# Kernel optimization log

Measured on AMD Instinct MI355X. Metric: run time of the kernel, lower is better.

## Reference

```python
import jax, jax.numpy as jnp
import numpy as np

V, E, S, B, T = 100000, 64, 4, 2048, 200
D = 2 * E          # memory_vector_dim
C = E              # controller_units
CIN = 2 * E + D    # controller input: x_t (2E) + prev read (D)
P = 2 * (D + 1) + 2 * D  # (key+beta) for read & write heads + erase + add


def setup_inputs() -> dict:
    key = jax.random.key(0)
    ks = jax.random.split(key, 16)
    g = lambda k, sh, sc=0.05: jax.random.normal(k, sh, dtype=jnp.float32) * sc
    return {
        "item": jax.random.randint(ks[0], (B,), 0, V),
        "cate": jax.random.randint(ks[1], (B,), 0, V),
        "hist_item": jax.random.randint(ks[2], (B, T), 0, V),
        "hist_cate": jax.random.randint(ks[3], (B, T), 0, V),
        "mask": jnp.ones((B, T), jnp.float32),
        "embedding": g(ks[4], (V, E)),
        "gru_Wih": g(ks[5], (3 * C, CIN)),
        "gru_Whh": g(ks[6], (3 * C, C)),
        "gru_bih": jnp.zeros((3 * C,), jnp.float32),
        "gru_bhh": jnp.zeros((3 * C,), jnp.float32),
        "Wp": g(ks[7], (P, C)),
        "bp": jnp.zeros((P,), jnp.float32),
        "Wo": g(ks[8], (E, C + D)),
        "bo": jnp.zeros((E,), jnp.float32),
        "M0": g(ks[9], (S, D), 0.1),
        "fc1_w": g(ks[10], (200, 5 * E)),
        "fc1_b": jnp.zeros((200,), jnp.float32),
        "prelu1_a": jnp.full((1,), 0.25, jnp.float32),
        "fc2_w": g(ks[11], (80, 200)),
        "fc2_b": jnp.zeros((80,), jnp.float32),
        "prelu2_a": jnp.full((1,), 0.25, jnp.float32),
        "fc3_w": g(ks[12], (2, 80)),
        "fc3_b": jnp.zeros((2,), jnp.float32),
    }


def _cos_addr(k, beta, M):
    # content addressing: softmax(beta * cosine_sim(k, M))  k:[B,D] M:[B,S,D]
    kn = k / (jnp.linalg.norm(k, axis=-1, keepdims=True) + 1e-8)
    Mn = M / (jnp.linalg.norm(M, axis=-1, keepdims=True) + 1e-8)
    K = jnp.einsum('bd,bsd->bs', kn, Mn)
    return jax.nn.softmax(beta[:, None] * K, axis=-1)


def _prelu(x, a):
    return jnp.where(x > 0, x, a * x)


def _mimn_rnn(hist_emb, mask, gru_Wih, gru_Whh, gru_bih, gru_bhh, Wp, bp, Wo, bo, M0):
    Bn = hist_emb.shape[0]
    h0 = jnp.zeros((Bn, C), hist_emb.dtype)
    r0 = jnp.zeros((Bn, D), hist_emb.dtype)
    Mi = jnp.broadcast_to(M0[None], (Bn, S, D))

    def step(carry, inp):
        h, M, read = carry
        x_t, m_t = inp                      # x_t [B,2E], m_t [B]
        ctrl_in = jnp.concatenate([x_t, read], axis=-1)
        gi = ctrl_in @ gru_Wih.T + gru_bih
        gh = h @ gru_Whh.T + gru_bhh
        i_r, i_z, i_n = jnp.split(gi, 3, axis=-1)
        h_r, h_z, h_n = jnp.split(gh, 3, axis=-1)
        rg = jax.nn.sigmoid(i_r + h_r)
        zg = jax.nn.sigmoid(i_z + h_z)
        ng = jnp.tanh(i_n + rg * h_n)
        h_new = (1.0 - zg) * ng + zg * h
        # head parameters
        p = h_new @ Wp.T + bp               # [B, P]
        hp_r, hp_w = p[:, :D + 1], p[:, D + 1:2 * (D + 1)]
        erase = jax.nn.sigmoid(p[:, 2 * (D + 1):2 * (D + 1) + D])
        add = jnp.tanh(p[:, -D:])
        k_r, beta_r = jnp.tanh(hp_r[:, :D]), jax.nn.softplus(hp_r[:, D])
        k_w, beta_w = jnp.tanh(hp_w[:, :D]), jax.nn.softplus(hp_w[:, D])
        w_r = _cos_addr(k_r, beta_r, M)
        w_w = _cos_addr(k_w, beta_w, M)
        read_new = jnp.einsum('bs,bsd->bd', w_r, M)
        M_new = M * (1.0 - w_w[..., None] * erase[:, None, :]) + w_w[..., None] * add[:, None, :]
        out = jnp.concatenate([h_new, read_new], axis=-1) @ Wo.T + bo  # [B,E]
        # sequence-length masking (dynamic_rnn semantics)
        v = (m_t > 0)[:, None]
        h = jnp.where(v, h_new, h)
        read = jnp.where(v, read_new, read)
        M = jnp.where(v[..., None], M_new, M)
        out = jnp.where(v, out, jnp.zeros_like(out))
        return (h, M, read), out

    xs = (jnp.swapaxes(hist_emb, 0, 1), jnp.swapaxes(mask, 0, 1))  # [T,B,...]
    _, outs = jax.lax.scan(step, (h0, Mi, r0), xs)
    return jnp.swapaxes(outs, 0, 1)  # [B,T,E]


def reference(item, cate, hist_item, hist_cate, mask, embedding,
              gru_Wih, gru_Whh, gru_bih, gru_bhh, Wp, bp, Wo, bo, M0,
              fc1_w, fc1_b, prelu1_a, fc2_w, fc2_b, prelu2_a, fc3_w, fc3_b):
    item_emb = jnp.concatenate([embedding[item], embedding[cate]], axis=1)      # [B,2E]
    hist_emb = jnp.concatenate([embedding[hist_item], embedding[hist_cate]], axis=2)  # [B,T,2E]
    seq_len = mask.sum(1).astype(jnp.int32)
    outputs = _mimn_rnn(hist_emb, mask, gru_Wih, gru_Whh, gru_bih, gru_bhh, Wp, bp, Wo, bo, M0)
    last_out = jnp.take_along_axis(outputs, (seq_len - 1)[:, None, None], axis=1)[:, 0, :]
    hist_sum = (hist_emb * mask[..., None]).sum(1)                              # [B,2E]
    x = jnp.concatenate([item_emb, hist_sum, last_out], axis=1)                 # [B,5E]
    x = _prelu(x @ fc1_w.T + fc1_b, prelu1_a)
    x = _prelu(x @ fc2_w.T + fc2_b, prelu2_a)
    return x @ fc3_w.T + fc3_b
```

## Files before the change

kernel.cpp:

```cpp
#include <hip/hip_runtime.h>

#define VV 100000
#define BB 2048
#define TT 200
#define GG 192
#define PP 514
#define RPB 8
#define NBT 1563

typedef _Float16 half8 __attribute__((ext_vector_type(8)));
typedef float floatx4 __attribute__((ext_vector_type(4)));
#define MFMA16(a, b, c) __builtin_amdgcn_mfma_f32_16x16x32_f16((a), (b), (c), 0, 0, 0)

#define BARRIER_LDS() do { \
    __asm__ volatile("s_waitcnt lgkmcnt(0)" ::: "memory"); \
    __builtin_amdgcn_s_barrier(); } while (0)
#define WAIT_LDS() __asm__ volatile("s_waitcnt lgkmcnt(0)" ::: "memory")

__device__ __forceinline__ float fsigm(float x) { return 1.0f / (1.0f + __expf(-x)); }
__device__ __forceinline__ float ftanh(float x) {
    float e = __expf(2.0f * x);
    return 1.0f - 2.0f / (e + 1.0f);
}
__device__ __forceinline__ float fsoftplus(float x) {
    float e = __expf(-fabsf(x));
    return fmaxf(x, 0.0f) + __logf(1.0f + e);
}

#define DPP_ADD(x, ctrl, rmask) \
    ((x) + __int_as_float(__builtin_amdgcn_update_dpp( \
        0, __float_as_int(x), (ctrl), (rmask), 0xf, true)))
__device__ __forceinline__ float wsum64(float x) {
    x = DPP_ADD(x, 0x111, 0xf);
    x = DPP_ADD(x, 0x112, 0xf);
    x = DPP_ADD(x, 0x114, 0xf);
    x = DPP_ADD(x, 0x118, 0xf);
    x = DPP_ADD(x, 0x142, 0xa);
    x = DPP_ADD(x, 0x143, 0xc);
    return __int_as_float(__builtin_amdgcn_readlane(__float_as_int(x), 63));
}
__device__ __forceinline__ float dot4(float4 w, float4 a) {
    return w.x * a.x + w.y * a.y + w.z * a.z + w.w * a.w;
}

__global__ __launch_bounds__(256) void prep(
    const float* __restrict__ emb,
    const float* __restrict__ Wih,
    const float* __restrict__ bih,
    float* __restrict__ GIi, float* __restrict__ GIc)
{
    __shared__ __align__(16) _Float16 sE16[64 * 72];
    const int tid = threadIdx.x;
    const int wv = tid >> 6, lane = tid & 63;
    const int nlo = lane & 15, kg = lane >> 4;

    const int v0 = blockIdx.x * 64;
    for (int i = tid; i < 64 * 64; i += 256) {
        int vv = i >> 6, k = i & 63;
        int gv = v0 + vv;
        sE16[vv * 72 + k] = (gv < VV) ? (_Float16)emb[(size_t)gv * 64 + k]
                                      : (_Float16)0.f;
    }
    half8 WF[6][2];
    float bias[6];
#pragma unroll
    for (int j = 0; j < 6; ++j) {
        int pid = 6 * wv + j;
        int tb = pid / 12, nt = pid % 12;
        int n = nt * 16 + nlo;
#pragma unroll
        for (int kb = 0; kb < 2; ++kb) {
            half8 f;
#pragma unroll
            for (int q = 0; q < 8; ++q)
                f[q] = (_Float16)Wih[n * 256 + tb * 64 + kb * 32 + kg * 8 + q];
            WF[j][kb] = f;
        }
        bias[j] = tb ? 0.f : bih[n];
    }
    __syncthreads();
#pragma unroll
    for (int mt = 0; mt < 4; ++mt) {
        const int ar = (16 * mt + nlo) * 72 + 8 * kg;
        half8 a0 = *(const half8*)&sE16[ar];
        half8 a1 = *(const half8*)&sE16[ar + 32];
#pragma unroll
        for (int j = 0; j < 6; ++j) {
            floatx4 acc = {0.f, 0.f, 0.f, 0.f};
            acc = MFMA16(a0, WF[j][0], acc);
            acc = MFMA16(a1, WF[j][1], acc);
            int pid = 6 * wv + j;
            int tb = pid / 12, nt = pid % 12;
            float* dst = tb ? GIc : GIi;
            int n = nt * 16 + nlo;
#pragma unroll
            for (int q = 0; q < 4; ++q) {
                int gv = v0 + 16 * mt + 4 * kg + q;
                if (gv < VV) dst[(size_t)gv * GG + n] = acc[q] + bias[j];
            }
        }
    }
}

__global__ __attribute__((amdgpu_flat_work_group_size(512, 512))) void mimn_rnn(
    const int* __restrict__ item, const int* __restrict__ cate,
    const int* __restrict__ hist_item, const int* __restrict__ hist_cate,
    const float* __restrict__ mask,
    const float* __restrict__ Wih,
    const float* __restrict__ Whh,
    const float* __restrict__ bhh,
    const float* __restrict__ Wp,
    const float* __restrict__ bp,
    const float* __restrict__ Wo,
    const float* __restrict__ bo,
    const float* __restrict__ M0,
    const float* __restrict__ GIi, const float* __restrict__ GIc,
    const float* __restrict__ emb,
    const float* __restrict__ fc1w, const float* __restrict__ fc1b,
    const float* __restrict__ pa1,
    const float* __restrict__ fc2w, const float* __restrict__ fc2b,
    const float* __restrict__ pa2,
    const float* __restrict__ fc3w, const float* __restrict__ fc3b,
    float* __restrict__ out)
{
    __shared__ __align__(16) float sU[4160];
    __shared__ __align__(16) _Float16 act16[16 * 200];
    __shared__ __align__(16) _Float16 hn16[16 * 72];
    __shared__ float sHnF[RPB * 64];
    __shared__ float sWpT[2 * 64];
    __shared__ float sHist[RPB * 128];
    __shared__ float sLO[RPB * 64];
    __shared__ unsigned char sMaskB[RPB * TT];

    const int tid = threadIdx.x;
    const int b0 = blockIdx.x * RPB;
    const int wv = tid >> 6, lane = tid & 63;
    const int nlo = lane & 15, kg = lane >> 4;
    const bool hasN = wv >= 4;

    for (int i = tid; i < 16 * 200; i += 512) act16[i] = (_Float16)0.f;
    for (int i = tid; i < 16 * 72; i += 512) hn16[i] = (_Float16)0.f;
    for (int i = tid; i < RPB * 64; i += 512) sHnF[i] = 0.f;
    if (tid < 128) sWpT[tid] = Wp[512 * 64 + tid];
    for (int i = tid; i < RPB * TT; i += 512) {
        int r = i / TT, tt = i - r * TT;
        sMaskB[i] = (mask[(size_t)(b0 + r) * TT + tt] > 0.f) ? 1 : 0;
    }

    int ts;
    {
        const size_t base = (size_t)(b0 + wv) * TT;
        float accI = 0.f, accC = 0.f, msum = 0.f;
#pragma unroll 2
        for (int t = 0; t < TT; ++t) {
            float m = mask[base + t];
            int ii = hist_item[base + t];
            int ic = hist_cate[base + t];
            accI += m * emb[(size_t)ii * 64 + lane];
            accC += m * emb[(size_t)ic * 64 + lane];
            msum += m;
        }
        sHist[wv * 128 + lane] = accI;
        sHist[wv * 128 + 64 + lane] = accC;
        ts = (int)(msum + 0.5f) - 1;
        ts = ts < 0 ? 0 : (ts > TT - 1 ? TT - 1 : ts);
    }

    float hreg = 0.f;
    float M1[4], M2[4];
#pragma unroll
    for (int s = 0; s < 4; ++s) {
        M1[s] = M0[s * 128 + lane];
        M2[s] = M0[s * 128 + 64 + lane];
    }
    const float bhhRZ = bhh[16 * wv + nlo];
    const float bhhN  = hasN ? bhh[128 + 16 * (wv - 4) + nlo] : 0.f;
    float bpP[4];
#pragma unroll
    for (int i = 0; i < 4; ++i) bpP[i] = bp[16 * (wv + 8 * i) + nlo];
    const float bpT = (tid < 16) ? bp[512 + (tid >> 3)] : 0.f;

    half8 WG[6];
    {
        int n = 16 * wv + nlo;
#pragma unroll
        for (int kb = 0; kb < 6; ++kb) {
            half8 f;
#pragma unroll
            for (int j = 0; j < 8; ++j) {
                int k = 32 * kb + 8 * kg + j;
                float w = (k < 128) ? Wih[n * 256 + 128 + k] : Whh[n * 64 + (k - 128)];
                f[j] = (_Float16)w;
            }
            WG[kb] = f;
        }
    }
    half8 WN[6];
    if (hasN) {
        int n = 128 + 16 * (wv - 4) + nlo;
#pragma unroll
        for (int kb = 0; kb < 4; ++kb) {
            half8 f;
#pragma unroll
            for (int j = 0; j < 8; ++j) f[j] = (_Float16)Wih[n * 256 + 128 + 32 * kb + 8 * kg + j];
            WN[kb] = f;
        }
#pragma unroll
        for (int kb = 0; kb < 2; ++kb) {
            half8 f;
#pragma unroll
            for (int j = 0; j < 8; ++j) f[j] = (_Float16)Whh[n * 64 + 32 * kb + 8 * kg + j];
            WN[4 + kb] = f;
        }
    } else {
#pragma unroll
        for (int q = 0; q < 6; ++q) WN[q] = half8{};
    }
    half8 WP[8];
#pragma unroll
    for (int i = 0; i < 4; ++i) {
        int n = 16 * (wv + 8 * i) + nlo;
#pragma unroll
        for (int kb = 0; kb < 2; ++kb) {
            half8 f;
#pragma unroll
            for (int j = 0; j < 8; ++j) f[j] = (_Float16)Wp[n * 64 + 32 * kb + 8 * kg + j];
            WP[2 * i + kb] = f;
        }
    }

    float giA, giB, giC, gcA, gcB, gcC;
    {
        int ri = hist_item[(size_t)(b0 + wv) * TT];
        int rc = hist_cate[(size_t)(b0 + wv) * TT];
        giA = GIi[(size_t)ri * GG + lane];
        giB = GIi[(size_t)ri * GG + 64 + lane];
        giC = GIi[(size_t)ri * GG + 128 + lane];
        gcA = GIc[(size_t)rc * GG + lane];
        gcB = GIc[(size_t)rc * GG + 64 + lane];
        gcC = GIc[(size_t)rc * GG + 128 + lane];
    }
    float pKw1 = 0.f, pKw2 = 0.f, pBw = 0.f, pEr1 = 0.f, pEr2 = 0.f;
    float pAd1 = 0.f, pAd2 = 0.f;
    float nMs[4] = {1.f, 1.f, 1.f, 1.f};
    bool vldPrev = false;
    __syncthreads();

    for (int t = 0; t < TT; ++t) {
        {
            const int abase = nlo * 200 + 8 * kg;
            floatx4 accRZ = {0.f, 0.f, 0.f, 0.f};
            floatx4 accI = {0.f, 0.f, 0.f, 0.f};
            floatx4 accH = {0.f, 0.f, 0.f, 0.f};
            half8 a0 = *(const half8*)&act16[abase];
            half8 a1 = *(const half8*)&act16[abase + 32];
            half8 a2 = *(const half8*)&act16[abase + 64];
            accRZ = MFMA16(a0, WG[0], accRZ);
            accRZ = MFMA16(a1, WG[1], accRZ);
            accRZ = MFMA16(a2, WG[2], accRZ);
            if (hasN) {
                accI = MFMA16(a0, WN[0], accI);
                accI = MFMA16(a1, WN[1], accI);
                accI = MFMA16(a2, WN[2], accI);
            }
            a0 = *(const half8*)&act16[abase + 96];
            a1 = *(const half8*)&act16[abase + 128];
            a2 = *(const half8*)&act16[abase + 160];
            accRZ = MFMA16(a0, WG[3], accRZ);
            accRZ = MFMA16(a1, WG[4], accRZ);
            accRZ = MFMA16(a2, WG[5], accRZ);
            if (hasN) {
                accI = MFMA16(a0, WN[3], accI);
                accH = MFMA16(a1, WN[4], accH);
                accH = MFMA16(a2, WN[5], accH);
            }
            if (t > 0) {
                float kw1 = ftanh(pKw1), kw2 = ftanh(pKw2);
                float beta_w = fsoftplus(pBw);
                float nkw = sqrtf(wsum64(kw1 * kw1 + kw2 * kw2)) + 1e-8f;
                float Kw[4];
#pragma unroll
                for (int s = 0; s < 4; ++s) {
                    float dw = wsum64(kw1 * M1[s] + kw2 * M2[s]);
                    Kw[s] = dw / (nkw * nMs[s]);
                }
                float ww_[4];
                float mx = fmaxf(fmaxf(beta_w * Kw[0], beta_w * Kw[1]),
                                 fmaxf(beta_w * Kw[2], beta_w * Kw[3]));
                float sum = 0.f;
#pragma unroll
                for (int s = 0; s < 4; ++s) { ww_[s] = __expf(beta_w * Kw[s] - mx); sum += ww_[s]; }
                float inv = 1.f / sum;
                if (vldPrev) {
                    float er1 = fsigm(pEr1), er2 = fsigm(pEr2);
                    float ad1 = ftanh(pAd1), ad2 = ftanh(pAd2);
#pragma unroll
                    for (int s = 0; s < 4; ++s) {
                        float w = ww_[s] * inv;
                        M1[s] = M1[s] * (1.f - w * er1) + w * ad1;
                        M2[s] = M2[s] * (1.f - w * er2) + w * ad2;
                    }
                }
            }
            if (kg < 2) {
                int n = 16 * wv + nlo;
#pragma unroll
                for (int q = 0; q < 4; ++q) sU[(4 * kg + q) * 132 + n] = accRZ[q] + bhhRZ;
                if (hasN) {
                    int n64 = 16 * (wv - 4) + nlo;
#pragma unroll
                    for (int q = 0; q < 4; ++q) {
                        sU[1056 + (4 * kg + q) * 68 + n64] = accI[q];
                        sU[1600 + (4 * kg + q) * 68 + n64] = accH[q] + bhhN;
                    }
                }
            }
        }
        BARRIER_LDS();
        bool vld;
        {
            const int r = wv;
            float g_r = sU[r * 132 + lane] + giA + gcA;
            float g_z = sU[r * 132 + 64 + lane] + giB + gcB;
            float i_n = sU[1056 + r * 68 + lane] + giC + gcC;
            float h_n = sU[1600 + r * 68 + lane];
            float rg = fsigm(g_r);
            float zg = fsigm(g_z);
            float ng = ftanh(i_n + rg * h_n);
            float hn = (1.f - zg) * ng + zg * hreg;
            vld = sMaskB[r * TT + t] != 0;
            float hc = vld ? hn : hreg;
            hreg = hc;
            act16[r * 200 + 128 + lane] = (_Float16)hc;
            hn16[r * 72 + lane] = (_Float16)hn;
            sHnF[r * 64 + lane] = hn;
        }
        {
            int tn = (t + 1 < TT) ? t + 1 : TT - 1;
            int ri = hist_item[(size_t)(b0 + wv) * TT + tn];
            int rc = hist_cate[(size_t)(b0 + wv) * TT + tn];
            giA = GIi[(size_t)ri * GG + lane];
            giB = GIi[(size_t)ri * GG + 64 + lane];
            giC = GIi[(size_t)ri * GG + 128 + lane];
            gcA = GIc[(size_t)rc * GG + lane];
            gcB = GIc[(size_t)rc * GG + 64 + lane];
            gcC = GIc[(size_t)rc * GG + 128 + lane];
        }
        BARRIER_LDS();
        {
            const int bbase = nlo * 72 + 8 * kg;
            half8 b0f = *(const half8*)&hn16[bbase];
            half8 b1f = *(const half8*)&hn16[bbase + 32];
#pragma unroll
            for (int i = 0; i < 4; ++i) {
                floatx4 acc = {0.f, 0.f, 0.f, 0.f};
                acc = MFMA16(b0f, WP[2 * i], acc);
                acc = MFMA16(b1f, WP[2 * i + 1], acc);
                if (kg < 2) {
                    int n = 16 * (wv + 8 * i) + nlo;
#pragma unroll
                    for (int q = 0; q < 4; ++q) sU[(4 * kg + q) * 520 + n] = acc[q] + bpP[i];
                }
            }
        }
        if (tid < 16) {
            int r = tid & 7, j = tid >> 3;
            float acc = 0.f;
#pragma unroll
            for (int k = 0; k < 64; ++k) acc += sHnF[r * 64 + k] * sWpT[j * 64 + k];
            sU[r * 520 + 512 + j] = acc + bpT;
        }
        BARRIER_LDS();
        {
            const int row = wv;
            const int pb = row * 520;
#define PV(n) (sU[pb + (n)])
            float kr1 = ftanh(PV(lane)),       kr2 = ftanh(PV(64 + lane));
            float beta_r = fsoftplus(PV(128));
            pKw1 = PV(129 + lane); pKw2 = PV(193 + lane);
            pBw  = PV(257);
            pEr1 = PV(258 + lane); pEr2 = PV(322 + lane);
            pAd1 = PV(386 + lane); pAd2 = PV(450 + lane);
#undef PV
            float nkr = sqrtf(wsum64(kr1 * kr1 + kr2 * kr2)) + 1e-8f;
            float Kr[4];
#pragma unroll
            for (int s = 0; s < 4; ++s) {
                nMs[s] = sqrtf(wsum64(M1[s] * M1[s] + M2[s] * M2[s])) + 1e-8f;
                float dr = wsum64(kr1 * M1[s] + kr2 * M2[s]);
                Kr[s] = dr / (nkr * nMs[s]);
            }
            float wr_[4];
            {
                float mx = fmaxf(fmaxf(beta_r * Kr[0], beta_r * Kr[1]),
                                 fmaxf(beta_r * Kr[2], beta_r * Kr[3]));
                float sum = 0.f;
#pragma unroll
                for (int s = 0; s < 4; ++s) { wr_[s] = __expf(beta_r * Kr[s] - mx); sum += wr_[s]; }
                float inv = 1.f / sum;
#pragma unroll
                for (int s = 0; s < 4; ++s) wr_[s] *= inv;
            }
            float rn1 = 0.f, rn2 = 0.f;
#pragma unroll
            for (int s = 0; s < 4; ++s) { rn1 += wr_[s] * M1[s]; rn2 += wr_[s] * M2[s]; }
            vldPrev = vld;
            if (vld) {
                act16[row * 200 + lane]      = (_Float16)rn1;
                act16[row * 200 + 64 + lane] = (_Float16)rn2;
            }
            if (t == ts) {
                float* stash = &sU[pb];
                stash[lane] = rn1; stash[64 + lane] = rn2;
                WAIT_LDS();
                float acc = bo[lane];
                const float* wo = Wo + lane * GG;
                for (int k = 0; k < 64; ++k)  acc += sHnF[row * 64 + k] * wo[k];
                for (int k = 0; k < 128; ++k) acc += stash[k] * wo[64 + k];
                if (!vld) acc = 0.f;
                sLO[row * 64 + lane] = acc;
            }
        }
        BARRIER_LDS();
    }

    {
        const int row = wv;
        const int b = b0 + row;
        float* X  = &sU[row * 520];
        float* H1 = &sU[row * 520 + 320];
        int it = item[b], ct = cate[b];
        X[lane]       = emb[(size_t)it * 64 + lane];
        X[64 + lane]  = emb[(size_t)ct * 64 + lane];
        X[128 + lane] = sHist[row * 128 + lane];
        X[192 + lane] = sHist[row * 128 + 64 + lane];
        X[256 + lane] = sLO[row * 64 + lane];
        WAIT_LDS();
        float a1 = pa1[0];
        for (int o = lane; o < 200; o += 64) {
            const float4* w = (const float4*)(fc1w + o * 320);
            float acc = fc1b[o];
#pragma unroll
            for (int q = 0; q < 80; ++q) acc += dot4(w[q], *(const float4*)&X[q * 4]);
            H1[o] = acc > 0.f ? acc : a1 * acc;
        }
        WAIT_LDS();
        float a2 = pa2[0];
        for (int o = lane; o < 80; o += 64) {
            const float4* w = (const float4*)(fc2w + o * 200);
            float acc = fc2b[o];
#pragma unroll
            for (int q = 0; q < 50; ++q) acc += dot4(w[q], *(const float4*)&H1[q * 4]);
            X[o] = acc > 0.f ? acc : a2 * acc;
        }
        WAIT_LDS();
        if (lane < 2) {
            const float4* w = (const float4*)(fc3w + lane * 80);
            float acc = fc3b[lane];
#pragma unroll
            for (int q = 0; q < 20; ++q) acc += dot4(w[q], *(const float4*)&X[q * 4]);
            out[(size_t)b * 2 + lane] = acc;
        }
    }
}

extern "C" void kernel_launch(void* const* d_in, const int* in_sizes, int n_in,
                              void* d_out, int out_size, void* d_ws, size_t ws_size,
                              hipStream_t stream) {
    (void)in_sizes; (void)n_in; (void)out_size; (void)ws_size;
    const int*   item      = (const int*)d_in[0];
    const int*   cate      = (const int*)d_in[1];
    const int*   hist_item = (const int*)d_in[2];
    const int*   hist_cate = (const int*)d_in[3];
    const float* mask = (const float*)d_in[4];
    const float* emb  = (const float*)d_in[5];
    const float* Wih  = (const float*)d_in[6];
    const float* Whh  = (const float*)d_in[7];
    const float* bih  = (const float*)d_in[8];
    const float* bhh  = (const float*)d_in[9];
    const float* Wp   = (const float*)d_in[10];
    const float* bp   = (const float*)d_in[11];
    const float* Wo   = (const float*)d_in[12];
    const float* bo   = (const float*)d_in[13];
    const float* M0   = (const float*)d_in[14];
    const float* fc1w = (const float*)d_in[15];
    const float* fc1b = (const float*)d_in[16];
    const float* pa1  = (const float*)d_in[17];
    const float* fc2w = (const float*)d_in[18];
    const float* fc2b = (const float*)d_in[19];
    const float* pa2  = (const float*)d_in[20];
    const float* fc3w = (const float*)d_in[21];
    const float* fc3b = (const float*)d_in[22];

    float* GIi = (float*)d_ws;
    float* GIc = GIi + (size_t)VV * GG;

    prep<<<NBT, 256, 0, stream>>>(emb, Wih, bih, GIi, GIc);
    mimn_rnn<<<BB / RPB, 512, 0, stream>>>(item, cate, hist_item, hist_cate, mask,
                                           Wih, Whh, bhh, Wp, bp, Wo, bo, M0,
                                           GIi, GIc, emb,
                                           fc1w, fc1b, pa1, fc2w, fc2b, pa2,
                                           fc3w, fc3b, (float*)d_out);
}
```

Measured before the change: 1.111 ms.

## Move history-sum and sequence-length reduction into extra blocks of the prep kernel

The masked history embedding sum and sequence length were computed serially at the start of each RNN block, with one wave per row looping over 200 timesteps. They are now computed by 2048 extra blocks appended to the prep launch, each splitting a row across 4 waves by table and time half, and written to workspace. The RNN kernel reads the precomputed values, which shortens its serial prologue. The cost is extra global traffic and a larger prep grid, plus reliance on workspace capacity for the new buffers.

New measurement: 1.063 ms. 1.04x faster.

```diff
diff --git a/kernel.cpp b/kernel.cpp
--- a/kernel.cpp
+++ b/kernel.cpp
@@ -47,58 +47,86 @@
     const float* __restrict__ emb,
     const float* __restrict__ Wih,
     const float* __restrict__ bih,
-    float* __restrict__ GIi, float* __restrict__ GIc)
+    const int* __restrict__ hist_item, const int* __restrict__ hist_cate,
+    const float* __restrict__ mask,
+    float* __restrict__ GIi, float* __restrict__ GIc,
+    float* __restrict__ hist_sum, int* __restrict__ seqlen)
 {
     __shared__ __align__(16) _Float16 sE16[64 * 72];
     const int tid = threadIdx.x;
     const int wv = tid >> 6, lane = tid & 63;
     const int nlo = lane & 15, kg = lane >> 4;
 
-    const int v0 = blockIdx.x * 64;
-    for (int i = tid; i < 64 * 64; i += 256) {
-        int vv = i >> 6, k = i & 63;
-        int gv = v0 + vv;
-        sE16[vv * 72 + k] = (gv < VV) ? (_Float16)emb[(size_t)gv * 64 + k]
-                                      : (_Float16)0.f;
-    }
-    half8 WF[6][2];
-    float bias[6];
-#pragma unroll
-    for (int j = 0; j < 6; ++j) {
-        int pid = 6 * wv + j;
-        int tb = pid / 12, nt = pid % 12;
-        int n = nt * 16 + nlo;
-#pragma unroll
-        for (int kb = 0; kb < 2; ++kb) {
-            half8 f;
-#pragma unroll
-            for (int q = 0; q < 8; ++q)
-                f[q] = (_Float16)Wih[n * 256 + tb * 64 + kb * 32 + kg * 8 + q];
-            WF[j][kb] = f;
-        }
-        bias[j] = tb ? 0.f : bih[n];
-    }
-    __syncthreads();
-#pragma unroll
-    for (int mt = 0; mt < 4; ++mt) {
-        const int ar = (16 * mt + nlo) * 72 + 8 * kg;
-        half8 a0 = *(const half8*)&sE16[ar];
-        half8 a1 = *(const half8*)&sE16[ar + 32];
+    if (blockIdx.x < NBT) {
+        const int v0 = blockIdx.x * 64;
+        for (int i = tid; i < 64 * 64; i += 256) {
+            int vv = i >> 6, k = i & 63;
+            int gv = v0 + vv;
+            sE16[vv * 72 + k] = (gv < VV) ? (_Float16)emb[(size_t)gv * 64 + k]
+                                          : (_Float16)0.f;
+        }
+        half8 WF[6][2];
+        float bias[6];
 #pragma unroll
         for (int j = 0; j < 6; ++j) {
-            floatx4 acc = {0.f, 0.f, 0.f, 0.f};
-            acc = MFMA16(a0, WF[j][0], acc);
-            acc = MFMA16(a1, WF[j][1], acc);
             int pid = 6 * wv + j;
             int tb = pid / 12, nt = pid % 12;
-            float* dst = tb ? GIc : GIi;
             int n = nt * 16 + nlo;
 #pragma unroll
-            for (int q = 0; q < 4; ++q) {
-                int gv = v0 + 16 * mt + 4 * kg + q;
-                if (gv < VV) dst[(size_t)gv * GG + n] = acc[q] + bias[j];
-            }
-        }
+            for (int kb = 0; kb < 2; ++kb) {
+                half8 f;
+#pragma unroll
+                for (int q = 0; q < 8; ++q)
+                    f[q] = (_Float16)Wih[n * 256 + tb * 64 + kb * 32 + kg * 8 + q];
+                WF[j][kb] = f;
+            }
+            bias[j] = tb ? 0.f : bih[n];
+        }
+        __syncthreads();
+#pragma unroll
+        for (int mt = 0; mt < 4; ++mt) {
+            const int ar = (16 * mt + nlo) * 72 + 8 * kg;
+            half8 a0 = *(const half8*)&sE16[ar];
+            half8 a1 = *(const half8*)&sE16[ar + 32];
+#pragma unroll
+            for (int j = 0; j < 6; ++j) {
+                floatx4 acc = {0.f, 0.f, 0.f, 0.f};
+                acc = MFMA16(a0, WF[j][0], acc);
+                acc = MFMA16(a1, WF[j][1], acc);
+                int pid = 6 * wv + j;
+                int tb = pid / 12, nt = pid % 12;
+                float* dst = tb ? GIc : GIi;
+                int n = nt * 16 + nlo;
+#pragma unroll
+                for (int q = 0; q < 4; ++q) {
+                    int gv = v0 + 16 * mt + 4 * kg + q;
+                    if (gv < VV) dst[(size_t)gv * GG + n] = acc[q] + bias[j];
+                }
+            }
+        }
+    } else {
+        float* sP = (float*)sE16;
+        float* sM4 = sP + 256;
+        const int b = blockIdx.x - NBT;
+        const int* hidx = (wv & 2) ? hist_cate : hist_item;
+        const int t0 = (wv & 1) * (TT / 2);
+        const size_t base = (size_t)b * TT;
+        float acc = 0.f, msum = 0.f;
+        for (int t = t0; t < t0 + TT / 2; ++t) {
+            float m = mask[base + t];
+            int idx = hidx[base + t];
+            acc += m * emb[(size_t)idx * 64 + lane];
+            msum += m;
+        }
+        sP[wv * 64 + lane] = acc;
+        if (wv < 2 && lane == 0) sM4[wv] = msum;
+        __syncthreads();
+        if (tid < 128) {
+            int half = tid >> 6, l = tid & 63;
+            hist_sum[(size_t)b * 128 + half * 64 + l] =
+                sP[(half * 2) * 64 + l] + sP[(half * 2 + 1) * 64 + l];
+        }
+        if (tid == 0) seqlen[b] = (int)(sM4[0] + sM4[1] + 0.5f);
     }
 }
 
@@ -115,7 +143,9 @@
     const float* __restrict__ bo,
     const float* __restrict__ M0,
     const float* __restrict__ GIi, const float* __restrict__ GIc,
+    const int* __restrict__ seqlen,
     const float* __restrict__ emb,
+    const float* __restrict__ hist_sum,
     const float* __restrict__ fc1w, const float* __restrict__ fc1b,
     const float* __restrict__ pa1,
     const float* __restrict__ fc2w, const float* __restrict__ fc2b,
@@ -128,7 +158,6 @@
     __shared__ __align__(16) _Float16 hn16[16 * 72];
     __shared__ float sHnF[RPB * 64];
     __shared__ float sWpT[2 * 64];
-    __shared__ float sHist[RPB * 128];
     __shared__ float sLO[RPB * 64];
     __shared__ unsigned char sMaskB[RPB * TT];
 
@@ -147,25 +176,6 @@
         sMaskB[i] = (mask[(size_t)(b0 + r) * TT + tt] > 0.f) ? 1 : 0;
     }
 
-    int ts;
-    {
-        const size_t base = (size_t)(b0 + wv) * TT;
-        float accI = 0.f, accC = 0.f, msum = 0.f;
-#pragma unroll 2
-        for (int t = 0; t < TT; ++t) {
-            float m = mask[base + t];
-            int ii = hist_item[base + t];
-            int ic = hist_cate[base + t];
-            accI += m * emb[(size_t)ii * 64 + lane];
-            accC += m * emb[(size_t)ic * 64 + lane];
-            msum += m;
-        }
-        sHist[wv * 128 + lane] = accI;
-        sHist[wv * 128 + 64 + lane] = accC;
-        ts = (int)(msum + 0.5f) - 1;
-        ts = ts < 0 ? 0 : (ts > TT - 1 ? TT - 1 : ts);
-    }
-
     float hreg = 0.f;
     float M1[4], M2[4];
 #pragma unroll
@@ -228,6 +238,9 @@
             WP[2 * i + kb] = f;
         }
     }
+
+    int ts = seqlen[b0 + wv] - 1;
+    ts = ts < 0 ? 0 : (ts > TT - 1 ? TT - 1 : ts);
 
     float giA, giB, giC, gcA, gcB, gcC;
     {
@@ -432,8 +445,8 @@
         int it = item[b], ct = cate[b];
         X[lane]       = emb[(size_t)it * 64 + lane];
         X[64 + lane]  = emb[(size_t)ct * 64 + lane];
-        X[128 + lane] = sHist[row * 128 + lane];
-        X[192 + lane] = sHist[row * 128 + 64 + lane];
+        X[128 + lane] = hist_sum[(size_t)b * 128 + lane];
+        X[192 + lane] = hist_sum[(size_t)b * 128 + 64 + lane];
         X[256 + lane] = sLO[row * 64 + lane];
         WAIT_LDS();
         float a1 = pa1[0];
@@ -494,11 +507,14 @@
 
     float* GIi = (float*)d_ws;
     float* GIc = GIi + (size_t)VV * GG;
-
-    prep<<<NBT, 256, 0, stream>>>(emb, Wih, bih, GIi, GIc);
+    float* hist_sum = GIc + (size_t)VV * GG;
+    int* seqlen = (int*)(hist_sum + (size_t)BB * 128);
+
+    prep<<<NBT + BB, 256, 0, stream>>>(emb, Wih, bih, hist_item, hist_cate,
+                                       mask, GIi, GIc, hist_sum, seqlen);
     mimn_rnn<<<BB / RPB, 512, 0, stream>>>(item, cate, hist_item, hist_cate, mask,
                                            Wih, Whh, bhh, Wp, bp, Wo, bo, M0,
-                                           GIi, GIc, emb,
+                                           GIi, GIc, seqlen, emb, hist_sum,
                                            fc1w, fc1b, pa1, fc2w, fc2b, pa2,
                                            fc3w, fc3b, (float*)d_out);
 }
```
